# Kernel optimization log

Hardware: AMD Instinct MI355X
Metric: run time of the kernel (lower is better)

The kernel has to match this reference:

```python
import jax, jax.numpy as jnp
import numpy as np

T, N, L = 512, 128, 256           # encoder steps, batch, decode steps
KV, VS = 128, 128                 # key_size, value_size
EMB, HID, VOC = 256, 512, 34


def _lstm_cell(x, h, c, W_ih, W_hh, b_ih, b_hh):
    # PyTorch LSTMCell gate order: i, f, g, o
    g = x @ W_ih.T + b_ih + h @ W_hh.T + b_hh
    i, f, gg, o = jnp.split(g, 4, axis=-1)
    c2 = jax.nn.sigmoid(f) * c + jax.nn.sigmoid(i) * jnp.tanh(gg)
    h2 = jax.nn.sigmoid(o) * jnp.tanh(c2)
    return h2, c2


def setup_inputs() -> dict:
    k = jax.random.key(0)
    ks = jax.random.split(k, 16)
    s = 0.05
    return {
        "key": jax.random.normal(ks[0], (T, N, KV), jnp.float32),
        "values": jax.random.normal(ks[1], (T, N, VS), jnp.float32),
        "lens": jax.random.randint(ks[2], (N,), 1, T + 1),
        "text": jax.random.randint(ks[3], (N, L), 0, VOC),
        "emb": jax.random.normal(ks[4], (VOC, EMB), jnp.float32) * s,
        "W_ih1": jax.random.normal(ks[5], (4 * HID, EMB + VS), jnp.float32) * s,
        "W_hh1": jax.random.normal(ks[6], (4 * HID, HID), jnp.float32) * s,
        "b_ih1": jnp.zeros((4 * HID,), jnp.float32),
        "b_hh1": jnp.zeros((4 * HID,), jnp.float32),
        "W_ih2": jax.random.normal(ks[7], (4 * KV, HID), jnp.float32) * s,
        "W_hh2": jax.random.normal(ks[8], (4 * KV, KV), jnp.float32) * s,
        "b_ih2": jnp.zeros((4 * KV,), jnp.float32),
        "b_hh2": jnp.zeros((4 * KV,), jnp.float32),
        "W_out": jax.random.normal(ks[9], (VOC, KV + VS), jnp.float32) * s,
        "b_out": jnp.zeros((VOC,), jnp.float32),
    }


def reference(key, values, lens, text, emb, W_ih1, W_hh1, b_ih1, b_hh1,
              W_ih2, W_hh2, b_ih2, b_hh2, W_out, b_out):
    # key/values: (T, N, 128); teacher-forced decode over L steps.
    pad_mask = jnp.arange(T)[None, :] >= lens[:, None]        # (N, T)
    embs = emb[text]                                          # (N, L, EMB)
    embs = jnp.transpose(embs, (1, 0, 2))                     # (L, N, EMB)

    def step(carry, e_t):
        h1, c1, h2, c2, ctx = carry
        x = jnp.concatenate([e_t, ctx], axis=-1)
        h1, c1 = _lstm_cell(x, h1, c1, W_ih1, W_hh1, b_ih1, b_hh1)
        h2, c2 = _lstm_cell(h1, h2, c2, W_ih2, W_hh2, b_ih2, b_hh2)
        # masked bmm attention: energy (N, T)
        energy = jnp.einsum('tnk,nk->nt', key, h2)
        energy = jnp.where(pad_mask, -1e9, energy)
        attn = jax.nn.softmax(energy, axis=1)
        ctx = jnp.einsum('nt,tnv->nv', attn, values)
        pred = jnp.concatenate([h2, ctx], axis=-1) @ W_out.T + b_out
        return (h1, c1, h2, c2, ctx), pred

    init = (jnp.zeros((N, HID)), jnp.zeros((N, HID)),
            jnp.zeros((N, KV)), jnp.zeros((N, KV)),
            jnp.zeros((N, VS)))
    _, preds = jax.lax.scan(step, init, embs)                 # (L, N, VOC)
    return jnp.transpose(preds, (1, 0, 2))                    # (N, L, VOC)
```

## Files before the change

kernel.cpp:

```cpp
#include <hip/hip_runtime.h>
#include <hip/hip_cooperative_groups.h>
#include <math.h>

#define LDEC 256
#define VOCD 34
#define SPIN_MAX 2000000u
#define XSTR 660

typedef __attribute__((ext_vector_type(8))) short bf16x8;
typedef __attribute__((ext_vector_type(8))) unsigned short u16x8;
typedef __attribute__((ext_vector_type(4))) float f32x4;

#define OFF_W1H  0u
#define OFF_W1L  2621440u
#define OFF_W2H  5242880u
#define OFF_W2L  5898240u
#define OFF_EG   6553600u
#define OFF_B2   6832128u
#define OFF_WOT  6834176u
#define OFF_H1P  6868992u
#define OFF_H2P  7393280u
#define OFF_CTXP 7524352u
#define OFF_C1   7589888u
#define OFF_C2   7852032u
#define OFF_FLG  7917568u
#define OFF_KB   7919616u
#define OFF_VB   24696832u
#define WS_NEED  41474048u

__device__ __forceinline__ float sigf(float x) { return 1.0f / (1.0f + expf(-x)); }
__device__ __forceinline__ unsigned short f2b(float x) {
  unsigned int u = __float_as_uint(x);
  unsigned int r = (u + 0x7FFFu + ((u >> 16) & 1u)) >> 16;
  return (unsigned short)r;
}
__device__ __forceinline__ float b2f(unsigned short h) {
  return __uint_as_float(((unsigned int)h) << 16);
}
__device__ __forceinline__ unsigned packf(float x) {
  unsigned short hi = f2b(x);
  unsigned short lo = f2b(x - b2f(hi));
  return ((unsigned)hi << 16) | (unsigned)lo;
}
__device__ __forceinline__ float unpackf(unsigned p) {
  return b2f((unsigned short)(p >> 16)) + b2f((unsigned short)(p & 0xffffu));
}
__device__ __forceinline__ unsigned aload(const unsigned* p) {
  return __hip_atomic_load((unsigned*)p, __ATOMIC_RELAXED, __HIP_MEMORY_SCOPE_SYSTEM);
}
__device__ __forceinline__ void astore(unsigned* p, unsigned v) {
  __hip_atomic_store(p, v, __ATOMIC_RELAXED, __HIP_MEMORY_SCOPE_SYSTEM);
}
__device__ __forceinline__ void unpack8(const unsigned* p, bf16x8& xh, bf16x8& xl) {
#pragma unroll
  for (int j = 0; j < 8; j++) {
    unsigned v = p[j];
    xh[j] = (short)(v >> 16);
    xl[j] = (short)(v & 0xffffu);
  }
}

__device__ __forceinline__ void flag_arrive(unsigned* f) {
  __builtin_amdgcn_s_waitcnt(0);
  __hip_atomic_fetch_add(f, 1u, __ATOMIC_RELAXED, __HIP_MEMORY_SCOPE_SYSTEM);
}
__device__ __forceinline__ void flag_wait(unsigned* f, unsigned target, unsigned* budget) {
  if (*budget == 0) return;
  while (aload(f) < target) {
    __builtin_amdgcn_s_sleep(1);
    if (--(*budget) == 0) break;
  }
  asm volatile("" ::: "memory");
}

__global__ __launch_bounds__(256) void pack_w1(const float* __restrict__ Wih1,
                                               const float* __restrict__ Whh1,
                                               unsigned short* __restrict__ W1H,
                                               unsigned short* __restrict__ W1L) {
  int idx = blockIdx.x * 256 + threadIdx.x;
  int m = idx / 640, k = idx % 640;
  int u = m >> 2, q = m & 3;
  int g = q * 512 + u;
  float v = (k < 128) ? Wih1[g * 384 + 256 + k] : Whh1[g * 512 + (k - 128)];
  unsigned short hi = f2b(v);
  W1H[idx] = hi;
  W1L[idx] = f2b(v - b2f(hi));
}

__global__ __launch_bounds__(256) void pack_w2(const float* __restrict__ Wih2,
                                               const float* __restrict__ Whh2,
                                               unsigned short* __restrict__ W2H,
                                               unsigned short* __restrict__ W2L) {
  int idx = blockIdx.x * 256 + threadIdx.x;
  int m = idx / 640, k = idx % 640;
  int u = m >> 2, q = m & 3;
  int g = q * 128 + u;
  float v = (k < 512) ? Wih2[g * 512 + k] : Whh2[g * 128 + (k - 512)];
  unsigned short hi = f2b(v);
  W2H[idx] = hi;
  W2L[idx] = f2b(v - b2f(hi));
}

__global__ __launch_bounds__(256) void pack_eg(const float* __restrict__ emb,
                                               const float* __restrict__ Wih1,
                                               const float* __restrict__ bih1,
                                               const float* __restrict__ bhh1,
                                               float* __restrict__ EG) {
  int idx = blockIdx.x * 256 + threadIdx.x;
  int v = idx >> 11, m = idx & 2047;
  int u = m >> 2, q = m & 3;
  int g = q * 512 + u;
  float acc = bih1[g] + bhh1[g];
  const float* e = emb + v * 256;
  const float* w = Wih1 + g * 384;
  for (int k = 0; k < 256; k++) acc += e[k] * w[k];
  EG[idx] = acc;
}

__global__ __launch_bounds__(256) void pack_misc(const float* __restrict__ Wout,
                                                 const float* __restrict__ bih2,
                                                 const float* __restrict__ bhh2,
                                                 float* __restrict__ WoT,
                                                 float* __restrict__ B2) {
  int idx = blockIdx.x * 256 + threadIdx.x;
  if (idx < 8704) {
    int k = idx / 34, v = idx % 34;
    WoT[idx] = Wout[v * 256 + k];
  } else if (idx < 9216) {
    int m = idx - 8704;
    int u = m >> 2, q = m & 3;
    int g = q * 128 + u;
    B2[m] = bih2[g] + bhh2[g];
  }
}

__global__ __launch_bounds__(256) void pack_kv(const float* __restrict__ key,
                                               const float* __restrict__ values,
                                               unsigned short* __restrict__ KB,
                                               unsigned short* __restrict__ VB) {
  size_t idx = (size_t)blockIdx.x * 256 + threadIdx.x;
  KB[idx] = f2b(key[idx]);
  VB[idx] = f2b(values[idx]);
}

__device__ __forceinline__ void stage_h1(int gang, int tid, int rbuf,
                                         unsigned* xshA, const unsigned* __restrict__ H1P) {
  int kcol = tid & 15, nl = (tid >> 4) & 15, rep = tid >> 8;
  int n = gang * 16 + nl;
  const unsigned* h1p = H1P + rbuf * 65536 + n * 512;
#pragma unroll
  for (int j = 0; j < 10; j++) {
    int k = rep * 160 + j * 16 + kcol;
    if (k >= 128) xshA[nl * XSTR + k] = aload(h1p + (k - 128));
  }
}
__device__ __forceinline__ void stage_ctx(int gang, int tid,
                                          unsigned* xshA, const unsigned* __restrict__ CTXP) {
  int kcol = tid & 15, nl = (tid >> 4) & 15, rep = tid >> 8;
  int n = gang * 16 + nl;
  if (rep == 0) {
#pragma unroll
    for (int j = 0; j < 8; j++) {
      int k = j * 16 + kcol;
      xshA[nl * XSTR + k] = aload(CTXP + n * 128 + k);
    }
  }
}

__device__ __forceinline__ void A_compute(
    int gang, int gidx, int tid, int t, int wp,
    const unsigned* __restrict__ xshA, float* bred,
    const unsigned short* __restrict__ W1H, const unsigned short* __restrict__ W1L,
    const float* __restrict__ EG, const int* __restrict__ text,
    unsigned* __restrict__ H1P, float* __restrict__ C1)
{
  const int wid = tid >> 6, lane = tid & 63;
  const int l15 = lane & 15, lg = lane >> 4;
  const int gr = wid >> 2, gwid = wid & 3;
  const int kb0 = gwid * 160;
  const int mt = gidx * 4 + gr;

  {
    const unsigned short* whp = W1H + (size_t)(mt * 16 + l15) * 640 + kb0 + lg * 8;
    const unsigned short* wlp = W1L + (size_t)(mt * 16 + l15) * 640 + kb0 + lg * 8;
    const unsigned* xrow = xshA + l15 * XSTR + kb0 + lg * 8;
    f32x4 a0 = {0.0f, 0.0f, 0.0f, 0.0f};
    f32x4 a1 = {0.0f, 0.0f, 0.0f, 0.0f};
    f32x4 a2 = {0.0f, 0.0f, 0.0f, 0.0f};
#pragma unroll
    for (int ks = 0; ks < 5; ks++) {
      unsigned parr[8];
      *(uint4*)parr       = *(const uint4*)(xrow + ks * 32);
      *(uint4*)(parr + 4) = *(const uint4*)(xrow + ks * 32 + 4);
      bf16x8 xh_, xl_;
      unpack8(parr, xh_, xl_);
      bf16x8 wh_ = *(const bf16x8*)(whp + ks * 32);
      bf16x8 wl_ = *(const bf16x8*)(wlp + ks * 32);
      a0 = __builtin_amdgcn_mfma_f32_16x16x32_bf16(wh_, xh_, a0, 0, 0, 0);
      a1 = __builtin_amdgcn_mfma_f32_16x16x32_bf16(wl_, xh_, a1, 0, 0, 0);
      a2 = __builtin_amdgcn_mfma_f32_16x16x32_bf16(wh_, xl_, a2, 0, 0, 0);
    }
    f32x4 acc = a0 + a1;
    acc = acc + a2;
#pragma unroll
    for (int q = 0; q < 4; q++) bred[gr * 1024 + q * 256 + gwid * 64 + lane] = acc[q];
  }
  __syncthreads();

  if (gwid == 0) {
    const float* br = bred + gr * 1024;
    int n = gang * 16 + l15;
    int tok = text[n * LDEC + t];
    f32x4 egv = *(const f32x4*)(EG + (size_t)tok * 2048 + mt * 16 + lg * 4);
    float g0 = br[lane]       + br[64 + lane]  + br[128 + lane] + br[192 + lane] + egv[0];
    float g1 = br[256 + lane] + br[320 + lane] + br[384 + lane] + br[448 + lane] + egv[1];
    float g2 = br[512 + lane] + br[576 + lane] + br[640 + lane] + br[704 + lane] + egv[2];
    float g3 = br[768 + lane] + br[832 + lane] + br[896 + lane] + br[960 + lane] + egv[3];
    float ig = sigf(g0), fg = sigf(g1), gg = tanhf(g2), og = sigf(g3);
    int u = mt * 4 + lg;
    float c = fg * C1[u * 128 + n] + ig * gg;
    float h = og * tanhf(c);
    C1[u * 128 + n] = c;
    astore(H1P + wp * 65536 + n * 512 + u, packf(h));
  }
  __syncthreads();
}

__device__ __forceinline__ void dev_phaseB(
    int gang, int gidx, int tid, int rp, int wp, float* bred,
    const unsigned short* __restrict__ W2H, const unsigned short* __restrict__ W2L,
    const float* __restrict__ B2,
    const unsigned* __restrict__ H1P, unsigned* __restrict__ H2P,
    float* __restrict__ C2)
{
  const int wid = tid >> 6, lane = tid & 63;
  const int l15 = lane & 15, lg = lane >> 4;
  const int mtB = gidx;
  if (tid < 256) {
    const int kb0 = wid * 160;
    int n = gang * 16 + l15;
    const unsigned* x1 = H1P + wp * 65536 + n * 512;
    const unsigned* x2 = H2P + rp * 16384 + n * 128;
    const unsigned short* whp = W2H + (size_t)(mtB * 16 + l15) * 640 + kb0 + lg * 8;
    const unsigned short* wlp = W2L + (size_t)(mtB * 16 + l15) * 640 + kb0 + lg * 8;
    f32x4 a0 = {0.0f, 0.0f, 0.0f, 0.0f};
    f32x4 a1 = {0.0f, 0.0f, 0.0f, 0.0f};
    f32x4 a2 = {0.0f, 0.0f, 0.0f, 0.0f};
#pragma unroll
    for (int ks = 0; ks < 5; ks++) {
      int kb = kb0 + ks * 32;
      unsigned parr[8];
      const unsigned* src = (kb < 512) ? (x1 + kb + lg * 8) : (x2 + (kb - 512) + lg * 8);
#pragma unroll
      for (int j = 0; j < 8; j++) parr[j] = aload(src + j);
      bf16x8 xh_, xl_;
      unpack8(parr, xh_, xl_);
      bf16x8 wh_ = *(const bf16x8*)(whp + ks * 32);
      bf16x8 wl_ = *(const bf16x8*)(wlp + ks * 32);
      a0 = __builtin_amdgcn_mfma_f32_16x16x32_bf16(wh_, xh_, a0, 0, 0, 0);
      a1 = __builtin_amdgcn_mfma_f32_16x16x32_bf16(wl_, xh_, a1, 0, 0, 0);
      a2 = __builtin_amdgcn_mfma_f32_16x16x32_bf16(wh_, xl_, a2, 0, 0, 0);
    }
    f32x4 acc = a0 + a1;
    acc = acc + a2;
#pragma unroll
    for (int q = 0; q < 4; q++) bred[q * 256 + wid * 64 + lane] = acc[q];
  }
  __syncthreads();
  if (tid < 64) {
    f32x4 b2v = *(const f32x4*)(B2 + mtB * 16 + lg * 4);
    float g0 = bred[lane]       + bred[64 + lane]  + bred[128 + lane] + bred[192 + lane] + b2v[0];
    float g1 = bred[256 + lane] + bred[320 + lane] + bred[384 + lane] + bred[448 + lane] + b2v[1];
    float g2 = bred[512 + lane] + bred[576 + lane] + bred[640 + lane] + bred[704 + lane] + b2v[2];
    float g3 = bred[768 + lane] + bred[832 + lane] + bred[896 + lane] + bred[960 + lane] + b2v[3];
    int n = gang * 16 + l15;
    int u = mtB * 4 + lg;
    float c = sigf(g1) * C2[u * 128 + n] + sigf(g0) * tanhf(g2);
    float h = sigf(g3) * tanhf(c);
    C2[u * 128 + n] = c;
    astore(H2P + wp * 16384 + n * 128 + u, packf(h));
  }
  __syncthreads();
}

template <int BF16KV>
__device__ __forceinline__ void dev_phaseC(
    int n, int tid, int len, int t, int wp,
    float* cred, float* es, float* h2s, float* ctxs, float* pr, float* sred,
    const float* __restrict__ key, const float* __restrict__ values,
    const unsigned short* __restrict__ KB, const unsigned short* __restrict__ VB,
    const unsigned* __restrict__ H2P, const float* __restrict__ WoT,
    const float* __restrict__ bout, unsigned* __restrict__ CTXP,
    float* __restrict__ out)
{
  const int wid = tid >> 6, lane = tid & 63;
  if (tid < 128) h2s[tid] = unpackf(aload(H2P + wp * 16384 + n * 128 + tid));
  __syncthreads();
  float ls = 0.0f;
  if (tid < len) {
    float acc = 0.0f;
    if (BF16KV) {
      const u16x8* kr = (const u16x8*)(KB + ((size_t)tid * 128 + n) * 128);
#pragma unroll 4
      for (int k = 0; k < 16; k++) {
        u16x8 kv = kr[k];
#pragma unroll
        for (int j = 0; j < 8; j++) acc += b2f(kv[j]) * h2s[k * 8 + j];
      }
    } else {
      const float4* kr = (const float4*)(key + ((size_t)tid * 128 + n) * 128);
#pragma unroll 8
      for (int k = 0; k < 32; k++) {
        float4 kv = kr[k];
        acc += kv.x * h2s[4 * k] + kv.y * h2s[4 * k + 1] + kv.z * h2s[4 * k + 2] + kv.w * h2s[4 * k + 3];
      }
    }
    float p = expf(acc - 20.0f);
    es[tid] = p;
    ls = p;
  }
  ls += __shfl_xor(ls, 32); ls += __shfl_xor(ls, 16); ls += __shfl_xor(ls, 8);
  ls += __shfl_xor(ls, 4);  ls += __shfl_xor(ls, 2);  ls += __shfl_xor(ls, 1);
  if (lane == 0) sred[wid] = ls;
  __syncthreads();
  float S = 0.0f;
#pragma unroll
  for (int w = 0; w < 16; w++) S += sred[w];
  {
    int v4 = (tid & 31) * 4, tp = tid >> 5;
    float ax = 0.0f, ay = 0.0f, az = 0.0f, aw = 0.0f;
    if (BF16KV) {
#pragma unroll 2
      for (int tt = tp; tt < len; tt += 32) {
        float p = es[tt];
        const unsigned* w = (const unsigned*)(VB + ((size_t)tt * 128 + n) * 128 + v4);
        unsigned w0 = w[0], w1 = w[1];
        ax += p * b2f((unsigned short)(w0 & 0xffffu));
        ay += p * b2f((unsigned short)(w0 >> 16));
        az += p * b2f((unsigned short)(w1 & 0xffffu));
        aw += p * b2f((unsigned short)(w1 >> 16));
      }
    } else {
#pragma unroll 2
      for (int tt = tp; tt < len; tt += 32) {
        float p = es[tt];
        const float4 vv = *(const float4*)(values + ((size_t)tt * 128 + n) * 128 + v4);
        ax += p * vv.x; ay += p * vv.y; az += p * vv.z; aw += p * vv.w;
      }
    }
    float4 a4 = {ax, ay, az, aw};
    *(float4*)&cred[tp * 132 + v4] = a4;
  }
  __syncthreads();
  if (tid < 128) {
    float s4 = 0.0f;
#pragma unroll 8
    for (int tp2 = 0; tp2 < 32; tp2++) s4 += cred[tp2 * 132 + tid];
    float cv = s4 / S;
    ctxs[tid] = cv;
    astore(CTXP + n * 128 + tid, packf(cv));
  }
  __syncthreads();
  if (tid < 68) {
    int vv = tid % 34, part = tid / 34;
    const float* src = part ? ctxs : h2s;
    const float* wcol = WoT + (part ? 128 * 34 : 0);
    float a = 0.0f;
#pragma unroll 8
    for (int k2 = 0; k2 < 128; k2++) a += src[k2] * wcol[k2 * 34 + vv];
    pr[tid] = a;
  }
  __syncthreads();
  if (tid < 34) {
    out[(size_t)n * (LDEC * VOCD) + t * VOCD + tid] = bout[tid] + pr[tid] + pr[34 + tid];
  }
  __syncthreads();
}

__global__ void __launch_bounds__(1024, 1) kA(
    const unsigned short* __restrict__ W1H, const unsigned short* __restrict__ W1L,
    const float* __restrict__ EG, const int* __restrict__ text,
    const unsigned* __restrict__ CTXP, unsigned* __restrict__ H1P,
    float* __restrict__ C1, int t, int rp, int wp)
{
  __shared__ unsigned xshA[16 * XSTR];
  __shared__ float bred[4096];
  const int gang = blockIdx.x >> 5, gidx = blockIdx.x & 31;
  stage_h1(gang, threadIdx.x, rp, xshA, H1P);
  stage_ctx(gang, threadIdx.x, xshA, CTXP);
  __syncthreads();
  A_compute(gang, gidx, threadIdx.x, t, wp, xshA, bred, W1H, W1L, EG, text, H1P, C1);
}
__global__ void __launch_bounds__(256) kB(
    const unsigned short* __restrict__ W2H, const unsigned short* __restrict__ W2L,
    const float* __restrict__ B2, const unsigned* __restrict__ H1P,
    unsigned* __restrict__ H2P, float* __restrict__ C2, int rp, int wp)
{
  __shared__ float bred[1024];
  dev_phaseB(blockIdx.x >> 5, blockIdx.x & 31, threadIdx.x, rp, wp, bred,
             W2H, W2L, B2, H1P, H2P, C2);
}
template <int BF16KV>
__global__ void __launch_bounds__(1024, 1) kC(
    const float* __restrict__ key, const float* __restrict__ values,
    const unsigned short* __restrict__ KB, const unsigned short* __restrict__ VB,
    const int* __restrict__ lens, const unsigned* __restrict__ H2P,
    const float* __restrict__ WoT, const float* __restrict__ bout,
    unsigned* __restrict__ CTXP, float* __restrict__ out, int t, int wp)
{
  __shared__ float cred[4224];
  __shared__ float es[512];
  __shared__ float h2s[128];
  __shared__ float ctxs[128];
  __shared__ float pr[68];
  __shared__ float sred[16];
  int n = blockIdx.x;
  dev_phaseC<BF16KV>(n, threadIdx.x, lens[n], t, wp, cred, es, h2s, ctxs, pr, sred,
                     key, values, KB, VB, H2P, WoT, bout, CTXP, out);
}

template <int BF16KV>
__global__ void __launch_bounds__(1024, 1) decoder_coop(
    const float* __restrict__ key, const float* __restrict__ values,
    const unsigned short* __restrict__ KB, const unsigned short* __restrict__ VB,
    const int* __restrict__ lens, const int* __restrict__ text,
    const float* __restrict__ EG, const float* __restrict__ B2,
    const float* __restrict__ WoT, const float* __restrict__ bout,
    const unsigned short* __restrict__ W1H, const unsigned short* __restrict__ W1L,
    const unsigned short* __restrict__ W2H, const unsigned short* __restrict__ W2L,
    unsigned* __restrict__ CTXP, unsigned* __restrict__ H1P,
    unsigned* __restrict__ H2P, float* __restrict__ C1, float* __restrict__ C2,
    unsigned* __restrict__ FLG, float* __restrict__ out)
{
  __shared__ unsigned xshA[16 * XSTR];
  __shared__ float bred[4096];
  __shared__ float cred[4224];
  __shared__ float es[512];
  __shared__ float h2s[128];
  __shared__ float ctxs[128];
  __shared__ float pr[68];
  __shared__ float sred[16];

  const int bid = blockIdx.x, tid = threadIdx.x;
  const int gang = bid >> 5, gidx = bid & 31;
  unsigned* fA = FLG + gang * 16;
  unsigned* fB = FLG + 128 + gang * 16;
  unsigned* fC = FLG + 256 + gang * 16;
  const int cn = gang * 16 + gidx;
  const int clen = (gidx < 16) ? lens[cn] : 0;

  unsigned budget = SPIN_MAX;

  stage_h1(gang, tid, 1, xshA, H1P);

  for (int t = 0; t < LDEC; t++) {
    const int wp = t & 1, rp = (t + 1) & 1;

    stage_ctx(gang, tid, xshA, CTXP);
    __syncthreads();
    A_compute(gang, gidx, tid, t, wp, xshA, bred, W1H, W1L, EG, text, H1P, C1);
    if (tid == 0) { flag_arrive(fA); flag_wait(fA, 32u * (t + 1), &budget); }
    __syncthreads();

    stage_h1(gang, tid, wp, xshA, H1P);

    dev_phaseB(gang, gidx, tid, rp, wp, bred, W2H, W2L, B2, H1P, H2P, C2);
    if (tid == 0) flag_arrive(fB);

    if (gidx < 16) {
      if (tid == 0) flag_wait(fB, 32u * (t + 1), &budget);
      __syncthreads();
      dev_phaseC<BF16KV>(cn, tid, clen, t, wp, cred, es, h2s, ctxs, pr, sred,
                         key, values, KB, VB, H2P, WoT, bout, CTXP, out);
      if (tid == 0) flag_arrive(fC);
    }
    if (tid == 0) flag_wait(fC, 16u * (t + 1), &budget);
    __syncthreads();
  }

  if (tid == 0 && budget == 0) out[0] = 7.0e6f;
}

extern "C" void kernel_launch(void* const* d_in, const int* in_sizes, int n_in,
                              void* d_out, int out_size, void* d_ws, size_t ws_size,
                              hipStream_t stream) {
  const float* key    = (const float*)d_in[0];
  const float* values = (const float*)d_in[1];
  const int*   lens   = (const int*)d_in[2];
  const int*   text   = (const int*)d_in[3];
  const float* emb    = (const float*)d_in[4];
  const float* Wih1   = (const float*)d_in[5];
  const float* Whh1   = (const float*)d_in[6];
  const float* bih1   = (const float*)d_in[7];
  const float* bhh1   = (const float*)d_in[8];
  const float* Wih2   = (const float*)d_in[9];
  const float* Whh2   = (const float*)d_in[10];
  const float* bih2   = (const float*)d_in[11];
  const float* bhh2   = (const float*)d_in[12];
  const float* Wout   = (const float*)d_in[13];
  const float* bout   = (const float*)d_in[14];

  char* ws = (char*)d_ws;
  unsigned short* W1H = (unsigned short*)(ws + OFF_W1H);
  unsigned short* W1L = (unsigned short*)(ws + OFF_W1L);
  unsigned short* W2H = (unsigned short*)(ws + OFF_W2H);
  unsigned short* W2L = (unsigned short*)(ws + OFF_W2L);
  float* EG   = (float*)(ws + OFF_EG);
  float* B2   = (float*)(ws + OFF_B2);
  float* WoT  = (float*)(ws + OFF_WOT);
  unsigned* H1P  = (unsigned*)(ws + OFF_H1P);
  unsigned* H2P  = (unsigned*)(ws + OFF_H2P);
  unsigned* CTXP = (unsigned*)(ws + OFF_CTXP);
  float* C1   = (float*)(ws + OFF_C1);
  float* C2   = (float*)(ws + OFF_C2);
  unsigned* FLG = (unsigned*)(ws + OFF_FLG);
  unsigned short* KB = (unsigned short*)(ws + OFF_KB);
  unsigned short* VB = (unsigned short*)(ws + OFF_VB);
  float* out  = (float*)d_out;

  const bool use16 = (ws_size >= (size_t)WS_NEED);

  hipMemsetAsync(CTXP, 0, 65536, stream);
  hipMemsetAsync((char*)H1P + 262144, 0, 262144, stream);
  hipMemsetAsync((char*)H2P + 65536, 0, 65536, stream);
  hipMemsetAsync(C1,  0, 262144, stream);
  hipMemsetAsync(C2,  0, 65536, stream);
  hipMemsetAsync(FLG, 0, 2048, stream);

  pack_w1  <<<5120, 256, 0, stream>>>(Wih1, Whh1, W1H, W1L);
  pack_w2  <<<1280, 256, 0, stream>>>(Wih2, Whh2, W2H, W2L);
  pack_eg  <<<272,  256, 0, stream>>>(emb, Wih1, bih1, bhh1, EG);
  pack_misc<<<36,   256, 0, stream>>>(Wout, bih2, bhh2, WoT, B2);
  if (use16) pack_kv<<<32768, 256, 0, stream>>>(key, values, KB, VB);

  const void* coop_fn = use16 ? (const void*)decoder_coop<1>
                              : (const void*)decoder_coop<0>;

  int maxBlk = 0;
  hipError_t qerr = hipOccupancyMaxActiveBlocksPerMultiprocessor(
      &maxBlk, coop_fn, 1024, 0);
  bool coop_ok = (qerr == hipSuccess && maxBlk >= 1);

  if (coop_ok) {
    void* args[] = {
      (void*)&key, (void*)&values, (void*)&KB, (void*)&VB,
      (void*)&lens, (void*)&text,
      (void*)&EG, (void*)&B2, (void*)&WoT, (void*)&bout,
      (void*)&W1H, (void*)&W1L, (void*)&W2H, (void*)&W2L,
      (void*)&CTXP, (void*)&H1P, (void*)&H2P, (void*)&C1, (void*)&C2,
      (void*)&FLG, (void*)&out
    };
    hipError_t err = hipLaunchCooperativeKernel(coop_fn, dim3(256), dim3(1024),
                                                args, 0, stream);
    if (err == hipSuccess) return;
  }

  for (int t = 0; t < LDEC; t++) {
    const int wp = t & 1, rp = (t + 1) & 1;
    kA<<<256, 1024, 0, stream>>>(W1H, W1L, EG, text, CTXP, H1P, C1, t, rp, wp);
    kB<<<256, 256,  0, stream>>>(W2H, W2L, B2, H1P, H2P, C2, rp, wp);
    if (use16)
      kC<1><<<128, 1024, 0, stream>>>(key, values, KB, VB, lens, H2P, WoT, bout,
                                      CTXP, out, t, wp);
    else
      kC<0><<<128, 1024, 0, stream>>>(key, values, KB, VB, lens, H2P, WoT, bout,
                                      CTXP, out, t, wp);
  }
}
```

Measured before the change: 7.881 ms.

## Fuse LSTM2 into per-batch attention blocks and replace counter barriers with per-block flags

Removes the separate phase B (the second LSTM cell, computed with split-bf16 MFMA across all blocks) and its grid-wide barrier. Each attention block now computes the second LSTM cell for its own batch row in fp32 scalar FMAs, using a transposed fp32 W2, and keeps h2 and c2 in shared memory across steps. The atomic-counter barriers are replaced by per-block step flags that a few threads poll. This cuts one grid synchronisation per step, but each of the 128 active blocks now streams the whole 1.3MB W2 every step with scalar code while the other 128 blocks sit idle in that phase.

```diff
diff --git a/kernel.cpp b/kernel.cpp
--- a/kernel.cpp
+++ b/kernel.cpp
@@ -13,8 +13,7 @@
 
 #define OFF_W1H  0u
 #define OFF_W1L  2621440u
-#define OFF_W2H  5242880u
-#define OFF_W2L  5898240u
+#define OFF_W2T  5242880u
 #define OFF_EG   6553600u
 #define OFF_B2   6832128u
 #define OFF_WOT  6834176u
@@ -24,9 +23,9 @@
 #define OFF_C1   7589888u
 #define OFF_C2   7852032u
 #define OFF_FLG  7917568u
-#define OFF_KB   7919616u
-#define OFF_VB   24696832u
-#define WS_NEED  41474048u
+#define OFF_KB   7966720u
+#define OFF_VB   24743936u
+#define WS_NEED  41521152u
 
 __device__ __forceinline__ float sigf(float x) { return 1.0f / (1.0f + expf(-x)); }
 __device__ __forceinline__ unsigned short f2b(float x) {
@@ -58,19 +57,6 @@
     xh[j] = (short)(v >> 16);
     xl[j] = (short)(v & 0xffffu);
   }
-}
-
-__device__ __forceinline__ void flag_arrive(unsigned* f) {
-  __builtin_amdgcn_s_waitcnt(0);
-  __hip_atomic_fetch_add(f, 1u, __ATOMIC_RELAXED, __HIP_MEMORY_SCOPE_SYSTEM);
-}
-__device__ __forceinline__ void flag_wait(unsigned* f, unsigned target, unsigned* budget) {
-  if (*budget == 0) return;
-  while (aload(f) < target) {
-    __builtin_amdgcn_s_sleep(1);
-    if (--(*budget) == 0) break;
-  }
-  asm volatile("" ::: "memory");
 }
 
 __global__ __launch_bounds__(256) void pack_w1(const float* __restrict__ Wih1,
@@ -87,18 +73,12 @@
   W1L[idx] = f2b(v - b2f(hi));
 }
 
-__global__ __launch_bounds__(256) void pack_w2(const float* __restrict__ Wih2,
-                                               const float* __restrict__ Whh2,
-                                               unsigned short* __restrict__ W2H,
-                                               unsigned short* __restrict__ W2L) {
+__global__ __launch_bounds__(256) void pack_w2t(const float* __restrict__ Wih2,
+                                                const float* __restrict__ Whh2,
+                                                float* __restrict__ W2T) {
   int idx = blockIdx.x * 256 + threadIdx.x;
-  int m = idx / 640, k = idx % 640;
-  int u = m >> 2, q = m & 3;
-  int g = q * 128 + u;
-  float v = (k < 512) ? Wih2[g * 512 + k] : Whh2[g * 128 + (k - 512)];
-  unsigned short hi = f2b(v);
-  W2H[idx] = hi;
-  W2L[idx] = f2b(v - b2f(hi));
+  int k = idx >> 9, g = idx & 511;
+  W2T[idx] = (k < 512) ? Wih2[g * 512 + k] : Whh2[g * 128 + (k - 512)];
 }
 
 __global__ __launch_bounds__(256) void pack_eg(const float* __restrict__ emb,
@@ -226,76 +206,48 @@
   __syncthreads();
 }
 
-__device__ __forceinline__ void dev_phaseB(
-    int gang, int gidx, int tid, int rp, int wp, float* bred,
-    const unsigned short* __restrict__ W2H, const unsigned short* __restrict__ W2L,
-    const float* __restrict__ B2,
-    const unsigned* __restrict__ H1P, unsigned* __restrict__ H2P,
-    float* __restrict__ C2)
+template <int BF16KV>
+__device__ __forceinline__ void C2_compute(
+    int n, int nl, int tid, int len, int t,
+    const unsigned* __restrict__ xshA,
+    float* gred, float* cred, float* es, float* ctxs, float* pr, float* sred,
+    float* h2olds, float* c2s,
+    const float* __restrict__ W2T, const float* __restrict__ B2,
+    const float* __restrict__ key, const float* __restrict__ values,
+    const unsigned short* __restrict__ KB, const unsigned short* __restrict__ VB,
+    const float* __restrict__ WoT, const float* __restrict__ bout,
+    unsigned* __restrict__ CTXP, float* __restrict__ out)
 {
   const int wid = tid >> 6, lane = tid & 63;
-  const int l15 = lane & 15, lg = lane >> 4;
-  const int mtB = gidx;
-  if (tid < 256) {
-    const int kb0 = wid * 160;
-    int n = gang * 16 + l15;
-    const unsigned* x1 = H1P + wp * 65536 + n * 512;
-    const unsigned* x2 = H2P + rp * 16384 + n * 128;
-    const unsigned short* whp = W2H + (size_t)(mtB * 16 + l15) * 640 + kb0 + lg * 8;
-    const unsigned short* wlp = W2L + (size_t)(mtB * 16 + l15) * 640 + kb0 + lg * 8;
-    f32x4 a0 = {0.0f, 0.0f, 0.0f, 0.0f};
-    f32x4 a1 = {0.0f, 0.0f, 0.0f, 0.0f};
-    f32x4 a2 = {0.0f, 0.0f, 0.0f, 0.0f};
-#pragma unroll
-    for (int ks = 0; ks < 5; ks++) {
-      int kb = kb0 + ks * 32;
-      unsigned parr[8];
-      const unsigned* src = (kb < 512) ? (x1 + kb + lg * 8) : (x2 + (kb - 512) + lg * 8);
-#pragma unroll
-      for (int j = 0; j < 8; j++) parr[j] = aload(src + j);
-      bf16x8 xh_, xl_;
-      unpack8(parr, xh_, xl_);
-      bf16x8 wh_ = *(const bf16x8*)(whp + ks * 32);
-      bf16x8 wl_ = *(const bf16x8*)(wlp + ks * 32);
-      a0 = __builtin_amdgcn_mfma_f32_16x16x32_bf16(wh_, xh_, a0, 0, 0, 0);
-      a1 = __builtin_amdgcn_mfma_f32_16x16x32_bf16(wl_, xh_, a1, 0, 0, 0);
-      a2 = __builtin_amdgcn_mfma_f32_16x16x32_bf16(wh_, xl_, a2, 0, 0, 0);
-    }
-    f32x4 acc = a0 + a1;
-    acc = acc + a2;
-#pragma unroll
-    for (int q = 0; q < 4; q++) bred[q * 256 + wid * 64 + lane] = acc[q];
-  }
-  __syncthreads();
-  if (tid < 64) {
-    f32x4 b2v = *(const f32x4*)(B2 + mtB * 16 + lg * 4);
-    float g0 = bred[lane]       + bred[64 + lane]  + bred[128 + lane] + bred[192 + lane] + b2v[0];
-    float g1 = bred[256 + lane] + bred[320 + lane] + bred[384 + lane] + bred[448 + lane] + b2v[1];
-    float g2 = bred[512 + lane] + bred[576 + lane] + bred[640 + lane] + bred[704 + lane] + b2v[2];
-    float g3 = bred[768 + lane] + bred[832 + lane] + bred[896 + lane] + bred[960 + lane] + b2v[3];
-    int n = gang * 16 + l15;
-    int u = mtB * 4 + lg;
-    float c = sigf(g1) * C2[u * 128 + n] + sigf(g0) * tanhf(g2);
+
+  {
+    const unsigned* xrow = xshA + nl * XSTR;
+    int g = tid & 511, half = tid >> 9;
+    const float* wcol = W2T + (size_t)(half * 320) * 512 + g;
+    float acc = 0.0f;
+#pragma unroll 8
+    for (int k = 0; k < 320; k++) {
+      int kk = half * 320 + k;
+      float xv = (kk < 512) ? unpackf(xrow[128 + kk]) : h2olds[kk - 512];
+      acc += wcol[(size_t)k * 512] * xv;
+    }
+    gred[tid] = acc;
+  }
+  __syncthreads();
+  if (tid < 128) {
+    int u = tid;
+    f32x4 bq = *(const f32x4*)(B2 + u * 4);
+    float g0 = gred[u]       + gred[512 + u]       + bq[0];
+    float g1 = gred[128 + u] + gred[640 + u]       + bq[1];
+    float g2 = gred[256 + u] + gred[768 + u]       + bq[2];
+    float g3 = gred[384 + u] + gred[896 + u]       + bq[3];
+    float c = sigf(g1) * c2s[u] + sigf(g0) * tanhf(g2);
     float h = sigf(g3) * tanhf(c);
-    C2[u * 128 + n] = c;
-    astore(H2P + wp * 16384 + n * 128 + u, packf(h));
-  }
-  __syncthreads();
-}
-
-template <int BF16KV>
-__device__ __forceinline__ void dev_phaseC(
-    int n, int tid, int len, int t, int wp,
-    float* cred, float* es, float* h2s, float* ctxs, float* pr, float* sred,
-    const float* __restrict__ key, const float* __restrict__ values,
-    const unsigned short* __restrict__ KB, const unsigned short* __restrict__ VB,
-    const unsigned* __restrict__ H2P, const float* __restrict__ WoT,
-    const float* __restrict__ bout, unsigned* __restrict__ CTXP,
-    float* __restrict__ out)
-{
-  const int wid = tid >> 6, lane = tid & 63;
-  if (tid < 128) h2s[tid] = unpackf(aload(H2P + wp * 16384 + n * 128 + tid));
-  __syncthreads();
+    c2s[u] = c;
+    h2olds[u] = h;
+  }
+  __syncthreads();
+
   float ls = 0.0f;
   if (tid < len) {
     float acc = 0.0f;
@@ -305,14 +257,15 @@
       for (int k = 0; k < 16; k++) {
         u16x8 kv = kr[k];
 #pragma unroll
-        for (int j = 0; j < 8; j++) acc += b2f(kv[j]) * h2s[k * 8 + j];
+        for (int j = 0; j < 8; j++) acc += b2f(kv[j]) * h2olds[k * 8 + j];
       }
     } else {
       const float4* kr = (const float4*)(key + ((size_t)tid * 128 + n) * 128);
 #pragma unroll 8
       for (int k = 0; k < 32; k++) {
         float4 kv = kr[k];
-        acc += kv.x * h2s[4 * k] + kv.y * h2s[4 * k + 1] + kv.z * h2s[4 * k + 2] + kv.w * h2s[4 * k + 3];
+        acc += kv.x * h2olds[4 * k] + kv.y * h2olds[4 * k + 1]
+             + kv.z * h2olds[4 * k + 2] + kv.w * h2olds[4 * k + 3];
       }
     }
     float p = expf(acc - 20.0f);
@@ -363,7 +316,7 @@
   __syncthreads();
   if (tid < 68) {
     int vv = tid % 34, part = tid / 34;
-    const float* src = part ? ctxs : h2s;
+    const float* src = part ? ctxs : h2olds;
     const float* wcol = WoT + (part ? 128 * 34 : 0);
     float a = 0.0f;
 #pragma unroll 8
@@ -391,32 +344,33 @@
   __syncthreads();
   A_compute(gang, gidx, threadIdx.x, t, wp, xshA, bred, W1H, W1L, EG, text, H1P, C1);
 }
-__global__ void __launch_bounds__(256) kB(
-    const unsigned short* __restrict__ W2H, const unsigned short* __restrict__ W2L,
-    const float* __restrict__ B2, const unsigned* __restrict__ H1P,
-    unsigned* __restrict__ H2P, float* __restrict__ C2, int rp, int wp)
-{
-  __shared__ float bred[1024];
-  dev_phaseB(blockIdx.x >> 5, blockIdx.x & 31, threadIdx.x, rp, wp, bred,
-             W2H, W2L, B2, H1P, H2P, C2);
-}
+
 template <int BF16KV>
-__global__ void __launch_bounds__(1024, 1) kC(
+__global__ void __launch_bounds__(1024, 1) kC2(
     const float* __restrict__ key, const float* __restrict__ values,
     const unsigned short* __restrict__ KB, const unsigned short* __restrict__ VB,
-    const int* __restrict__ lens, const unsigned* __restrict__ H2P,
+    const int* __restrict__ lens,
+    const float* __restrict__ W2T, const float* __restrict__ B2,
     const float* __restrict__ WoT, const float* __restrict__ bout,
+    const unsigned* __restrict__ H1P, float* __restrict__ H2F, float* __restrict__ C2,
     unsigned* __restrict__ CTXP, float* __restrict__ out, int t, int wp)
 {
+  __shared__ unsigned xsh1[16 * XSTR];
+  __shared__ float gred[1024];
   __shared__ float cred[4224];
   __shared__ float es[512];
-  __shared__ float h2s[128];
   __shared__ float ctxs[128];
   __shared__ float pr[68];
   __shared__ float sred[16];
-  int n = blockIdx.x;
-  dev_phaseC<BF16KV>(n, threadIdx.x, lens[n], t, wp, cred, es, h2s, ctxs, pr, sred,
-                     key, values, KB, VB, H2P, WoT, bout, CTXP, out);
+  __shared__ float h2olds[128];
+  __shared__ float c2s[128];
+  const int n = blockIdx.x, tid = threadIdx.x;
+  if (tid < 512) xsh1[128 + tid] = aload(H1P + wp * 65536 + n * 512 + tid);
+  if (tid < 128) { h2olds[tid] = H2F[n * 128 + tid]; c2s[tid] = C2[n * 128 + tid]; }
+  __syncthreads();
+  C2_compute<BF16KV>(n, 0, tid, lens[n], t, xsh1, gred, cred, es, ctxs, pr, sred,
+                     h2olds, c2s, W2T, B2, key, values, KB, VB, WoT, bout, CTXP, out);
+  if (tid < 128) { H2F[n * 128 + tid] = h2olds[tid]; C2[n * 128 + tid] = c2s[tid]; }
 }
 
 template <int BF16KV>
@@ -427,58 +381,79 @@
     const float* __restrict__ EG, const float* __restrict__ B2,
     const float* __restrict__ WoT, const float* __restrict__ bout,
     const unsigned short* __restrict__ W1H, const unsigned short* __restrict__ W1L,
-    const unsigned short* __restrict__ W2H, const unsigned short* __restrict__ W2L,
+    const float* __restrict__ W2T,
     unsigned* __restrict__ CTXP, unsigned* __restrict__ H1P,
-    unsigned* __restrict__ H2P, float* __restrict__ C1, float* __restrict__ C2,
-    unsigned* __restrict__ FLG, float* __restrict__ out)
+    float* __restrict__ C1, unsigned* __restrict__ FLG, float* __restrict__ out)
 {
   __shared__ unsigned xshA[16 * XSTR];
   __shared__ float bred[4096];
+  __shared__ float gred[1024];
   __shared__ float cred[4224];
   __shared__ float es[512];
-  __shared__ float h2s[128];
   __shared__ float ctxs[128];
   __shared__ float pr[68];
   __shared__ float sred[16];
+  __shared__ float h2olds[128];
+  __shared__ float c2s[128];
+  __shared__ unsigned deadsh;
 
   const int bid = blockIdx.x, tid = threadIdx.x;
   const int gang = bid >> 5, gidx = bid & 31;
-  unsigned* fA = FLG + gang * 16;
-  unsigned* fB = FLG + 128 + gang * 16;
-  unsigned* fC = FLG + 256 + gang * 16;
+  unsigned* sA = FLG + gang * 1024;
+  unsigned* sC = FLG + 8192 + gang * 512;
   const int cn = gang * 16 + gidx;
   const int clen = (gidx < 16) ? lens[cn] : 0;
 
   unsigned budget = SPIN_MAX;
 
+  if (tid < 128) { h2olds[tid] = 0.0f; c2s[tid] = 0.0f; }
+  if (tid == 0) deadsh = 0u;
   stage_h1(gang, tid, 1, xshA, H1P);
+  __syncthreads();
 
   for (int t = 0; t < LDEC; t++) {
-    const int wp = t & 1, rp = (t + 1) & 1;
+    const int wp = t & 1;
+    const unsigned tv = (unsigned)(t + 1);
 
     stage_ctx(gang, tid, xshA, CTXP);
     __syncthreads();
     A_compute(gang, gidx, tid, t, wp, xshA, bred, W1H, W1L, EG, text, H1P, C1);
-    if (tid == 0) { flag_arrive(fA); flag_wait(fA, 32u * (t + 1), &budget); }
+    if (tid == 0) {
+      __builtin_amdgcn_s_waitcnt(0);
+      astore(sA + gidx * 32, tv);
+    }
+    if (tid < 32) {
+      unsigned* s = sA + tid * 32;
+      while (budget && aload(s) < tv) {
+        __builtin_amdgcn_s_sleep(1);
+        if (--budget == 0) deadsh = 1u;
+      }
+    }
     __syncthreads();
 
     stage_h1(gang, tid, wp, xshA, H1P);
-
-    dev_phaseB(gang, gidx, tid, rp, wp, bred, W2H, W2L, B2, H1P, H2P, C2);
-    if (tid == 0) flag_arrive(fB);
+    __syncthreads();
 
     if (gidx < 16) {
-      if (tid == 0) flag_wait(fB, 32u * (t + 1), &budget);
-      __syncthreads();
-      dev_phaseC<BF16KV>(cn, tid, clen, t, wp, cred, es, h2s, ctxs, pr, sred,
-                         key, values, KB, VB, H2P, WoT, bout, CTXP, out);
-      if (tid == 0) flag_arrive(fC);
-    }
-    if (tid == 0) flag_wait(fC, 16u * (t + 1), &budget);
+      C2_compute<BF16KV>(cn, gidx, tid, clen, t, xshA, gred, cred, es, ctxs, pr,
+                         sred, h2olds, c2s, W2T, B2, key, values, KB, VB,
+                         WoT, bout, CTXP, out);
+      if (tid == 0) {
+        __builtin_amdgcn_s_waitcnt(0);
+        astore(sC + gidx * 32, tv);
+      }
+    }
+    if (tid < 16) {
+      unsigned* s = sC + tid * 32;
+      while (budget && aload(s) < tv) {
+        __builtin_amdgcn_s_sleep(1);
+        if (--budget == 0) deadsh = 1u;
+      }
+    }
     __syncthreads();
   }
 
-  if (tid == 0 && budget == 0) out[0] = 7.0e6f;
+  if (tid == 0 && deadsh) out[0] = 7.0e6f;
 }
 
 extern "C" void kernel_launch(void* const* d_in, const int* in_sizes, int n_in,
@@ -503,13 +478,12 @@
   char* ws = (char*)d_ws;
   unsigned short* W1H = (unsigned short*)(ws + OFF_W1H);
   unsigned short* W1L = (unsigned short*)(ws + OFF_W1L);
-  unsigned short* W2H = (unsigned short*)(ws + OFF_W2H);
-  unsigned short* W2L = (unsigned short*)(ws + OFF_W2L);
+  float* W2T  = (float*)(ws + OFF_W2T);
   float* EG   = (float*)(ws + OFF_EG);
   float* B2   = (float*)(ws + OFF_B2);
   float* WoT  = (float*)(ws + OFF_WOT);
   unsigned* H1P  = (unsigned*)(ws + OFF_H1P);
-  unsigned* H2P  = (unsigned*)(ws + OFF_H2P);
+  float* H2F  = (float*)(ws + OFF_H2P);
   unsigned* CTXP = (unsigned*)(ws + OFF_CTXP);
   float* C1   = (float*)(ws + OFF_C1);
   float* C2   = (float*)(ws + OFF_C2);
@@ -522,13 +496,13 @@
 
   hipMemsetAsync(CTXP, 0, 65536, stream);
   hipMemsetAsync((char*)H1P + 262144, 0, 262144, stream);
-  hipMemsetAsync((char*)H2P + 65536, 0, 65536, stream);
+  hipMemsetAsync(H2F, 0, 65536, stream);
   hipMemsetAsync(C1,  0, 262144, stream);
   hipMemsetAsync(C2,  0, 65536, stream);
-  hipMemsetAsync(FLG, 0, 2048, stream);
+  hipMemsetAsync(FLG, 0, 49152, stream);
 
   pack_w1  <<<5120, 256, 0, stream>>>(Wih1, Whh1, W1H, W1L);
-  pack_w2  <<<1280, 256, 0, stream>>>(Wih2, Whh2, W2H, W2L);
+  pack_w2t <<<1280, 256, 0, stream>>>(Wih2, Whh2, W2T);
   pack_eg  <<<272,  256, 0, stream>>>(emb, Wih1, bih1, bhh1, EG);
   pack_misc<<<36,   256, 0, stream>>>(Wout, bih2, bhh2, WoT, B2);
   if (use16) pack_kv<<<32768, 256, 0, stream>>>(key, values, KB, VB);
@@ -546,9 +520,8 @@
       (void*)&key, (void*)&values, (void*)&KB, (void*)&VB,
       (void*)&lens, (void*)&text,
       (void*)&EG, (void*)&B2, (void*)&WoT, (void*)&bout,
-      (void*)&W1H, (void*)&W1L, (void*)&W2H, (void*)&W2L,
-      (void*)&CTXP, (void*)&H1P, (void*)&H2P, (void*)&C1, (void*)&C2,
-      (void*)&FLG, (void*)&out
+      (void*)&W1H, (void*)&W1L, (void*)&W2T,
+      (void*)&CTXP, (void*)&H1P, (void*)&C1, (void*)&FLG, (void*)&out
     };
     hipError_t err = hipLaunchCooperativeKernel(coop_fn, dim3(256), dim3(1024),
                                                 args, 0, stream);
@@ -558,12 +531,11 @@
   for (int t = 0; t < LDEC; t++) {
     const int wp = t & 1, rp = (t + 1) & 1;
     kA<<<256, 1024, 0, stream>>>(W1H, W1L, EG, text, CTXP, H1P, C1, t, rp, wp);
-    kB<<<256, 256,  0, stream>>>(W2H, W2L, B2, H1P, H2P, C2, rp, wp);
     if (use16)
-      kC<1><<<128, 1024, 0, stream>>>(key, values, KB, VB, lens, H2P, WoT, bout,
-                                      CTXP, out, t, wp);
+      kC2<1><<<128, 1024, 0, stream>>>(key, values, KB, VB, lens, W2T, B2, WoT, bout,
+                                       H1P, H2F, C2, CTXP, out, t, wp);
     else
-      kC<0><<<128, 1024, 0, stream>>>(key, values, KB, VB, lens, H2P, WoT, bout,
-                                      CTXP, out, t, wp);
-  }
-}
+      kC2<0><<<128, 1024, 0, stream>>>(key, values, KB, VB, lens, W2T, B2, WoT, bout,
+                                       H1P, H2F, C2, CTXP, out, t, wp);
+  }
+}
```

Result: slower. 14.85 ms (+88.4%).

## Replace atomic-counter gang barriers with per-block epoch flags polled in parallel

Applied to the files above, without the earlier changes.

Swaps the shared fetch_add counter barriers for one epoch flag per block, each padded to its own 64-byte slot. The first 32 (or 16) threads each poll one flag, so arrivals no longer contend on a single atomic and waiting lanes check all peers at once. Phase B's flag publish now comes before staging h1, so staging overlaps the wait. Deadlock detection moves to a shared flag, and the workspace grows to hold the larger flag arrays.

```diff
diff --git a/kernel.cpp b/kernel.cpp
--- a/kernel.cpp
+++ b/kernel.cpp
@@ -24,9 +24,9 @@
 #define OFF_C1   7589888u
 #define OFF_C2   7852032u
 #define OFF_FLG  7917568u
-#define OFF_KB   7919616u
-#define OFF_VB   24696832u
-#define WS_NEED  41474048u
+#define OFF_KB   7966720u
+#define OFF_VB   24743936u
+#define WS_NEED  41521152u
 
 __device__ __forceinline__ float sigf(float x) { return 1.0f / (1.0f + expf(-x)); }
 __device__ __forceinline__ unsigned short f2b(float x) {
@@ -58,19 +58,6 @@
     xh[j] = (short)(v >> 16);
     xl[j] = (short)(v & 0xffffu);
   }
-}
-
-__device__ __forceinline__ void flag_arrive(unsigned* f) {
-  __builtin_amdgcn_s_waitcnt(0);
-  __hip_atomic_fetch_add(f, 1u, __ATOMIC_RELAXED, __HIP_MEMORY_SCOPE_SYSTEM);
-}
-__device__ __forceinline__ void flag_wait(unsigned* f, unsigned target, unsigned* budget) {
-  if (*budget == 0) return;
-  while (aload(f) < target) {
-    __builtin_amdgcn_s_sleep(1);
-    if (--(*budget) == 0) break;
-  }
-  asm volatile("" ::: "memory");
 }
 
 __global__ __launch_bounds__(256) void pack_w1(const float* __restrict__ Wih1,
@@ -440,45 +427,68 @@
   __shared__ float ctxs[128];
   __shared__ float pr[68];
   __shared__ float sred[16];
+  __shared__ unsigned deadsh;
 
   const int bid = blockIdx.x, tid = threadIdx.x;
   const int gang = bid >> 5, gidx = bid & 31;
-  unsigned* fA = FLG + gang * 16;
-  unsigned* fB = FLG + 128 + gang * 16;
-  unsigned* fC = FLG + 256 + gang * 16;
+  unsigned* sA = FLG + gang * 512;
+  unsigned* sB = FLG + 4096 + gang * 512;
+  unsigned* sC = FLG + 8192 + gang * 256;
   const int cn = gang * 16 + gidx;
   const int clen = (gidx < 16) ? lens[cn] : 0;
 
   unsigned budget = SPIN_MAX;
+  if (tid == 0) deadsh = 0u;
 
   stage_h1(gang, tid, 1, xshA, H1P);
+  __syncthreads();
 
   for (int t = 0; t < LDEC; t++) {
     const int wp = t & 1, rp = (t + 1) & 1;
+    const unsigned tv = (unsigned)(t + 1);
 
     stage_ctx(gang, tid, xshA, CTXP);
     __syncthreads();
     A_compute(gang, gidx, tid, t, wp, xshA, bred, W1H, W1L, EG, text, H1P, C1);
-    if (tid == 0) { flag_arrive(fA); flag_wait(fA, 32u * (t + 1), &budget); }
+    if (tid == 0) { __builtin_amdgcn_s_waitcnt(0); astore(sA + gidx * 16, tv); }
+    if (tid < 32) {
+      unsigned* s = sA + tid * 16;
+      while (aload(s) < tv) {
+        __builtin_amdgcn_s_sleep(1);
+        if (--budget == 0) { deadsh = 1u; break; }
+      }
+    }
     __syncthreads();
 
+    dev_phaseB(gang, gidx, tid, rp, wp, bred, W2H, W2L, B2, H1P, H2P, C2);
+    if (tid == 0) { __builtin_amdgcn_s_waitcnt(0); astore(sB + gidx * 16, tv); }
+
     stage_h1(gang, tid, wp, xshA, H1P);
 
-    dev_phaseB(gang, gidx, tid, rp, wp, bred, W2H, W2L, B2, H1P, H2P, C2);
-    if (tid == 0) flag_arrive(fB);
-
     if (gidx < 16) {
-      if (tid == 0) flag_wait(fB, 32u * (t + 1), &budget);
+      if (tid < 32) {
+        unsigned* s = sB + tid * 16;
+        while (aload(s) < tv) {
+          __builtin_amdgcn_s_sleep(1);
+          if (--budget == 0) { deadsh = 1u; break; }
+        }
+      }
       __syncthreads();
       dev_phaseC<BF16KV>(cn, tid, clen, t, wp, cred, es, h2s, ctxs, pr, sred,
                          key, values, KB, VB, H2P, WoT, bout, CTXP, out);
-      if (tid == 0) flag_arrive(fC);
-    }
-    if (tid == 0) flag_wait(fC, 16u * (t + 1), &budget);
+      if (tid == 0) { __builtin_amdgcn_s_waitcnt(0); astore(sC + gidx * 16, tv); }
+    }
+    if (tid < 16) {
+      unsigned* s = sC + tid * 16;
+      while (aload(s) < tv) {
+        __builtin_amdgcn_s_sleep(1);
+        if (--budget == 0) { deadsh = 1u; break; }
+      }
+    }
     __syncthreads();
   }
 
-  if (tid == 0 && budget == 0) out[0] = 7.0e6f;
+  if (tid == 0 && deadsh) out[0] = 7.0e6f;
 }
 
 extern "C" void kernel_launch(void* const* d_in, const int* in_sizes, int n_in,
@@ -525,7 +535,7 @@
   hipMemsetAsync((char*)H2P + 65536, 0, 65536, stream);
   hipMemsetAsync(C1,  0, 262144, stream);
   hipMemsetAsync(C2,  0, 65536, stream);
-  hipMemsetAsync(FLG, 0, 2048, stream);
+  hipMemsetAsync(FLG, 0, 49152, stream);
 
   pack_w1  <<<5120, 256, 0, stream>>>(Wih1, Whh1, W1H, W1L);
   pack_w2  <<<1280, 256, 0, stream>>>(Wih2, Whh2, W2H, W2L);
```

After: 7.875 ms. No clear change (-0.1%).
